# Optimization experiments

Measured on AMD Instinct MI355X. Metric: run time of the kernel, lower is better.

The kernel has to match this reference:

```python
import jax, jax.numpy as jnp
import numpy as np

DIST_THRESH = 150.0
ROW_EPS = 1e-6
BN_EPS = 1e-5


def setup_inputs() -> dict:
    key = jax.random.key(0)
    ks = jax.random.split(key, 6)
    B, N, T, D = 64, 64, 16, 512
    person_features = jax.random.normal(ks[0], (B, N, T, D), dtype=jnp.float32)
    # bboxes in pixel-ish units so the 150px threshold gives a mixed adjacency
    bboxes = jax.random.uniform(ks[1], (B, N, 4), dtype=jnp.float32) * 300.0
    w1 = jax.random.normal(ks[2], (D, D), dtype=jnp.float32) * (1.0 / np.sqrt(D))
    b1 = jax.random.normal(ks[3], (D,), dtype=jnp.float32) * 0.02
    w2 = jax.random.normal(ks[4], (D, D), dtype=jnp.float32) * (1.0 / np.sqrt(D))
    b2 = jax.random.normal(ks[5], (D,), dtype=jnp.float32) * 0.02
    g1 = jnp.ones((D,), jnp.float32); beta1 = jnp.zeros((D,), jnp.float32)
    g2 = jnp.ones((D,), jnp.float32); beta2 = jnp.zeros((D,), jnp.float32)
    return {"person_features": person_features, "bboxes": bboxes,
            "w1": w1, "b1": b1, "g1": g1, "beta1": beta1,
            "w2": w2, "b2": b2, "g2": g2, "beta2": beta2}


def _build_adjacency(bboxes):
    # centers: (B, N, 2) from x+w/2, y+h/2
    cx = bboxes[..., 0] + 0.5 * bboxes[..., 2]
    cy = bboxes[..., 1] + 0.5 * bboxes[..., 3]
    centers = jnp.stack([cx, cy], axis=-1)
    # pairwise distances (B, N, N), vectorized (replaces B*N*N python loop)
    diff = centers[:, :, None, :] - centers[:, None, :, :]
    dist = jnp.sqrt(jnp.sum(diff * diff, axis=-1))
    N = bboxes.shape[1]
    eye = jnp.eye(N, dtype=bboxes.dtype)
    off_diag = (eye[None] == 0.0)
    A = jnp.where((dist < DIST_THRESH) & off_diag, 1.0, 0.0) + eye[None]
    return A


def _stgcn(x, A, w, b, g, beta):
    # x: (B, N, C); A: (B, N, N)
    # torch: A_norm = A / (A.sum(dim=1 of A[i] -> axis=2) + eps)
    A_norm = A / (jnp.sum(A, axis=2, keepdims=True) + ROW_EPS)
    # x_graph = x[b].T @ A_norm[b]  -> (B, C, N)
    y = jnp.einsum('bnc,bnm->bcm', x, A_norm)
    # 1x1 conv == channel GEMM, bias added per out-channel
    y = jnp.einsum('oc,bcm->bom', w, y) + b[None, :, None]
    # BatchNorm2d in training mode: biased stats over (batch, spatial)
    mean = jnp.mean(y, axis=(0, 2), keepdims=True)
    var = jnp.mean(jnp.square(y - mean), axis=(0, 2), keepdims=True)
    y = (y - mean) / jnp.sqrt(var + BN_EPS)
    y = y * g[None, :, None] + beta[None, :, None]
    y = jax.nn.relu(y)
    return jnp.swapaxes(y, 1, 2)  # (B, N, C)


def reference(person_features, bboxes, w1, b1, g1, beta1, w2, b2, g2, beta2):
    A = _build_adjacency(bboxes)
    x = person_features[:, :, -1, :]  # (B, N, D) last frame
    h = _stgcn(x, A, w1, b1, g1, beta1)
    h = _stgcn(h, A, w2, b2, g2, beta2)
    # write enhanced features back into last timestep
    return person_features.at[:, :, -1, :].set(h)
```

## Files before the change

kernel.cpp:

```cpp
#include <hip/hip_runtime.h>
#include <hip/hip_bf16.h>


typedef __attribute__((ext_vector_type(8))) short short8;
typedef __attribute__((ext_vector_type(4))) float v4f;

#define DIST_THRESH 150.0f
#define ROW_EPS 1e-6f
#define BN_EPS 1e-5f

__device__ __forceinline__ ushort f2bf(float f) {
  union { __hip_bfloat16 h; ushort u; } cv;
  cv.h = __float2bfloat16(f);
  return cv.u;
}

__global__ __launch_bounds__(256) void k_copy_prep(const float4* __restrict__ in,
                                                   float4* __restrict__ out,
                                                   const float* __restrict__ w1,
                                                   const float* __restrict__ w2,
                                                   ushort* __restrict__ wb,
                                                   float* __restrict__ stats) {
  int blk = blockIdx.x;
  int t = threadIdx.x;
  if (blk < 8192) {
    size_t base = (size_t)blk * 1024 + t;
    float4 r0 = in[base];
    float4 r1 = in[base + 256];
    float4 r2 = in[base + 512];
    float4 r3 = in[base + 768];
    out[base] = r0;
    out[base + 256] = r1;
    out[base + 512] = r2;
    out[base + 768] = r3;
  } else {
    int idx = (blk - 8192) * 256 + t;
    float v = (idx < 262144) ? w1[idx] : w2[idx - 262144];
    wb[idx] = f2bf(v);
    if (idx < 2048) stats[idx] = 0.f;
  }
}

__global__ __launch_bounds__(256) void k_agg(const float* __restrict__ Xbase,
                                             int rowStride,
                                             const float* __restrict__ bb,
                                             const float* __restrict__ stats,
                                             const float* __restrict__ g,
                                             const float* __restrict__ beta,
                                             int applyBN,
                                             ushort* __restrict__ Z) {
  int b = blockIdx.x;
  int c0 = blockIdx.y * 128;
  int t = threadIdx.x;
  __shared__ float Xs[64][128];
  __shared__ float As[64][64];
  __shared__ float cxs[64], cys[64];
  __shared__ float scaleS[128], shiftS[128];
  __shared__ float rsum[64][4];
  __shared__ float invr[64];

  if (t < 64) {
    float4 v = *(const float4*)&bb[(size_t)(b * 64 + t) * 4];
    cxs[t] = v.x + 0.5f * v.z;
    cys[t] = v.y + 0.5f * v.w;
  }
  if (applyBN && t < 32) {
    int c = t * 4;
    float4 sm = *(const float4*)&stats[c0 + c];
    float4 sq = *(const float4*)&stats[512 + c0 + c];
    float4 gg = *(const float4*)&g[c0 + c];
    float4 bt = *(const float4*)&beta[c0 + c];
    const float inv = 1.0f / 4096.0f;
    float mean, var, sc;
    mean = sm.x * inv; var = sq.x * inv - mean * mean; sc = gg.x * rsqrtf(var + BN_EPS);
    scaleS[c] = sc; shiftS[c] = bt.x - mean * sc;
    mean = sm.y * inv; var = sq.y * inv - mean * mean; sc = gg.y * rsqrtf(var + BN_EPS);
    scaleS[c + 1] = sc; shiftS[c + 1] = bt.y - mean * sc;
    mean = sm.z * inv; var = sq.z * inv - mean * mean; sc = gg.z * rsqrtf(var + BN_EPS);
    scaleS[c + 2] = sc; shiftS[c + 2] = bt.z - mean * sc;
    mean = sm.w * inv; var = sq.w * inv - mean * mean; sc = gg.w * rsqrtf(var + BN_EPS);
    scaleS[c + 3] = sc; shiftS[c + 3] = bt.w - mean * sc;
  }
  __syncthreads();

  int an = t >> 2, aq = t & 3;
  float av[16];
  {
    float mycx = cxs[an], mycy = cys[an];
    float ps = 0.f;
#pragma unroll
    for (int j = 0; j < 16; ++j) {
      int m = aq * 16 + j;
      float dx = mycx - cxs[m], dy = mycy - cys[m];
      float d = sqrtf(dx * dx + dy * dy);
      float a = (m == an) ? 1.0f : ((d < DIST_THRESH) ? 1.0f : 0.0f);
      av[j] = a;
      ps += a;
    }
    rsum[an][aq] = ps;
  }

  const float* xb = Xbase + (size_t)b * 64 * rowStride;
  for (int i = t; i < 2048; i += 256) {
    int n = i >> 5, c4 = (i & 31) << 2;
    float4 x = *(const float4*)&xb[(size_t)n * rowStride + c0 + c4];
    if (applyBN) {
      x.x = fmaxf(x.x * scaleS[c4] + shiftS[c4], 0.f);
      x.y = fmaxf(x.y * scaleS[c4 + 1] + shiftS[c4 + 1], 0.f);
      x.z = fmaxf(x.z * scaleS[c4 + 2] + shiftS[c4 + 2], 0.f);
      x.w = fmaxf(x.w * scaleS[c4 + 3] + shiftS[c4 + 3], 0.f);
    }
    *(float4*)&Xs[n][c4] = x;
  }
  __syncthreads();

  if (t < 64)
    invr[t] = 1.0f / (rsum[t][0] + rsum[t][1] + rsum[t][2] + rsum[t][3] + ROW_EPS);
  __syncthreads();

  {
    float iv = invr[an];
#pragma unroll
    for (int j = 0; j < 16; ++j) As[an][aq * 16 + j] = av[j] * iv;
  }
  __syncthreads();

  int c4 = (t & 31) << 2;
  int m0 = (t >> 5) << 3;
  float4 acc[8];
#pragma unroll
  for (int i = 0; i < 8; ++i) acc[i] = make_float4(0.f, 0.f, 0.f, 0.f);

  for (int n = 0; n < 64; ++n) {
    float4 x = *(const float4*)&Xs[n][c4];
    float4 a0 = *(const float4*)&As[n][m0];
    float4 a1 = *(const float4*)&As[n][m0 + 4];
    float as[8] = {a0.x, a0.y, a0.z, a0.w, a1.x, a1.y, a1.z, a1.w};
#pragma unroll
    for (int i = 0; i < 8; ++i) {
      acc[i].x = fmaf(as[i], x.x, acc[i].x);
      acc[i].y = fmaf(as[i], x.y, acc[i].y);
      acc[i].z = fmaf(as[i], x.z, acc[i].z);
      acc[i].w = fmaf(as[i], x.w, acc[i].w);
    }
  }

  size_t zbase = (size_t)b * 64 * 512 + c0 + c4;
#pragma unroll
  for (int i = 0; i < 8; ++i) {
    int m = m0 + i;
    ushort4 zz;
    zz.x = f2bf(acc[i].x);
    zz.y = f2bf(acc[i].y);
    zz.z = f2bf(acc[i].z);
    zz.w = f2bf(acc[i].w);
    *(ushort4*)&Z[zbase + (size_t)m * 512] = zz;
  }
}

__global__ __launch_bounds__(256) void k_gemm(const ushort* __restrict__ Z,
                                              const ushort* __restrict__ W,
                                              const float* __restrict__ bias,
                                              float* __restrict__ Y,
                                              float* __restrict__ sum,
                                              float* __restrict__ sumsq) {
  __shared__ __align__(16) ushort Zs[64 * 40];
  __shared__ __align__(16) ushort Ws[64 * 40];
  __shared__ float redS[4][64], redQ[4][64];

  int t = threadIdx.x;
  int r0 = blockIdx.x * 64;
  int o0 = blockIdx.y * 64;
  int wv = t >> 6, lane = t & 63;
  int m = lane & 15, q = lane >> 4;

  v4f acc[4];
#pragma unroll
  for (int nf = 0; nf < 4; ++nf) acc[nf] = (v4f){0.f, 0.f, 0.f, 0.f};

  int srow = t >> 2, scg = (t & 3) << 3;
  const ushort* zp = &Z[(size_t)(r0 + srow) * 512 + scg];
  const ushort* wp = &W[(size_t)(o0 + srow) * 512 + scg];

  uint4 zv = *(const uint4*)zp;
  uint4 wvv = *(const uint4*)wp;

  for (int ks = 0; ks < 16; ++ks) {
    __syncthreads();
    *(uint4*)&Zs[srow * 40 + scg] = zv;
    *(uint4*)&Ws[srow * 40 + scg] = wvv;
    __syncthreads();

    if (ks < 15) {
      zv = *(const uint4*)(zp + (ks + 1) * 32);
      wvv = *(const uint4*)(wp + (ks + 1) * 32);
    }

    short8 a = *(const short8*)&Zs[(wv * 16 + m) * 40 + q * 8];
#pragma unroll
    for (int nf = 0; nf < 4; ++nf) {
      short8 bfr = *(const short8*)&Ws[(nf * 16 + m) * 40 + q * 8];
      acc[nf] = __builtin_amdgcn_mfma_f32_16x16x32_bf16(a, bfr, acc[nf], 0, 0, 0);
    }
  }

#pragma unroll
  for (int nf = 0; nf < 4; ++nf) {
    int col = o0 + nf * 16 + m;
    float bv = bias[col];
    float s = 0.f, s2 = 0.f;
#pragma unroll
    for (int reg = 0; reg < 4; ++reg) {
      int row = r0 + wv * 16 + q * 4 + reg;
      float y = acc[nf][reg] + bv;
      Y[(size_t)row * 512 + col] = y;
      s += y;
      s2 += y * y;
    }
    s += __shfl_xor(s, 16);
    s += __shfl_xor(s, 32);
    s2 += __shfl_xor(s2, 16);
    s2 += __shfl_xor(s2, 32);
    if (q == 0) {
      redS[wv][nf * 16 + m] = s;
      redQ[wv][nf * 16 + m] = s2;
    }
  }
  __syncthreads();
  if (t < 64) {
    float s = redS[0][t] + redS[1][t] + redS[2][t] + redS[3][t];
    float s2 = redQ[0][t] + redQ[1][t] + redQ[2][t] + redQ[3][t];
    atomicAdd(&sum[o0 + t], s);
    atomicAdd(&sumsq[o0 + t], s2);
  }
}

__global__ __launch_bounds__(256) void k_norm(const float* __restrict__ Y,
                                              const float* __restrict__ sum,
                                              const float* __restrict__ sumsq,
                                              const float* __restrict__ g,
                                              const float* __restrict__ beta,
                                              float* __restrict__ out) {
  int idx = blockIdx.x * 256 + threadIdx.x;
  int o = (idx & 127) << 2;
  int r = idx >> 7;
  float4 y = *(const float4*)&Y[(size_t)r * 512 + o];
  float4 sm = *(const float4*)&sum[o];
  float4 sq = *(const float4*)&sumsq[o];
  float4 gg = *(const float4*)&g[o];
  float4 bb = *(const float4*)&beta[o];
  const float inv = 1.0f / 4096.0f;
  float4 h;
  {
    float mean = sm.x * inv, var = sq.x * inv - mean * mean;
    h.x = fmaxf(gg.x * (y.x - mean) * rsqrtf(var + BN_EPS) + bb.x, 0.f);
  }
  {
    float mean = sm.y * inv, var = sq.y * inv - mean * mean;
    h.y = fmaxf(gg.y * (y.y - mean) * rsqrtf(var + BN_EPS) + bb.y, 0.f);
  }
  {
    float mean = sm.z * inv, var = sq.z * inv - mean * mean;
    h.z = fmaxf(gg.z * (y.z - mean) * rsqrtf(var + BN_EPS) + bb.z, 0.f);
  }
  {
    float mean = sm.w * inv, var = sq.w * inv - mean * mean;
    h.w = fmaxf(gg.w * (y.w - mean) * rsqrtf(var + BN_EPS) + bb.w, 0.f);
  }
  *(float4*)&out[((size_t)r * 16 + 15) * 512 + o] = h;
}

extern "C" void kernel_launch(void* const* d_in, const int* in_sizes, int n_in,
                              void* d_out, int out_size, void* d_ws, size_t ws_size,
                              hipStream_t stream) {
  const float* pf = (const float*)d_in[0];
  const float* bboxes = (const float*)d_in[1];
  const float* w1 = (const float*)d_in[2];
  const float* b1 = (const float*)d_in[3];
  const float* g1 = (const float*)d_in[4];
  const float* be1 = (const float*)d_in[5];
  const float* w2 = (const float*)d_in[6];
  const float* b2 = (const float*)d_in[7];
  const float* g2 = (const float*)d_in[8];
  const float* be2 = (const float*)d_in[9];
  float* out = (float*)d_out;

  ushort* wb = (ushort*)d_ws;
  ushort* Zb = wb + 524288;
  float* Yb = (float*)(Zb + 2097152);
  float* stats = Yb + 2097152;
  float* sum1 = stats;
  float* sq1 = stats + 512;
  float* sum2 = stats + 1024;
  float* sq2 = stats + 1536;

  k_copy_prep<<<10240, 256, 0, stream>>>((const float4*)pf, (float4*)out, w1, w2, wb, stats);

  k_agg<<<dim3(64, 4), 256, 0, stream>>>(pf + 7680, 8192, bboxes, stats, g1, be1, 0, Zb);
  k_gemm<<<dim3(64, 8), 256, 0, stream>>>(Zb, wb, b1, Yb, sum1, sq1);

  k_agg<<<dim3(64, 4), 256, 0, stream>>>(Yb, 512, bboxes, stats, g1, be1, 1, Zb);
  k_gemm<<<dim3(64, 8), 256, 0, stream>>>(Zb, wb + 262144, b2, Yb, sum2, sq2);

  k_norm<<<2048, 256, 0, stream>>>(Yb, sum2, sq2, g2, be2, out);
}
```

Measured before the change: 295.7 us.

## Fold feature copy and weight prep into compute kernels as extra blocks

Removes the standalone copy/prep kernel. Its 8192 copy slabs are split across the two aggregation and two GEMM launches as extra trailing blocks, and the bf16 weight conversion plus stats zeroing move into the first aggregation launch, now vectorised to float4. The goal is to overlap the bandwidth-bound copy of the feature tensor with the small, latency-bound graph and GEMM kernels, and to save one launch. The risk is that copy blocks inherit the compute kernels' large shared-memory footprint, which lowers their occupancy, and they compete with the compute blocks for bandwidth.

```diff
diff --git a/kernel.cpp b/kernel.cpp
--- a/kernel.cpp
+++ b/kernel.cpp
@@ -15,30 +15,18 @@
   return cv.u;
 }
 
-__global__ __launch_bounds__(256) void k_copy_prep(const float4* __restrict__ in,
-                                                   float4* __restrict__ out,
-                                                   const float* __restrict__ w1,
-                                                   const float* __restrict__ w2,
-                                                   ushort* __restrict__ wb,
-                                                   float* __restrict__ stats) {
-  int blk = blockIdx.x;
-  int t = threadIdx.x;
-  if (blk < 8192) {
-    size_t base = (size_t)blk * 1024 + t;
-    float4 r0 = in[base];
-    float4 r1 = in[base + 256];
-    float4 r2 = in[base + 512];
-    float4 r3 = in[base + 768];
-    out[base] = r0;
-    out[base + 256] = r1;
-    out[base + 512] = r2;
-    out[base + 768] = r3;
-  } else {
-    int idx = (blk - 8192) * 256 + t;
-    float v = (idx < 262144) ? w1[idx] : w2[idx - 262144];
-    wb[idx] = f2bf(v);
-    if (idx < 2048) stats[idx] = 0.f;
-  }
+__device__ __forceinline__ void copy_slab(const float4* __restrict__ in,
+                                          float4* __restrict__ out,
+                                          int blk, int t) {
+  size_t base = (size_t)blk * 1024 + t;
+  float4 r0 = in[base];
+  float4 r1 = in[base + 256];
+  float4 r2 = in[base + 512];
+  float4 r3 = in[base + 768];
+  out[base] = r0;
+  out[base + 256] = r1;
+  out[base + 512] = r2;
+  out[base + 768] = r3;
 }
 
 __global__ __launch_bounds__(256) void k_agg(const float* __restrict__ Xbase,
@@ -48,10 +36,38 @@
                                              const float* __restrict__ g,
                                              const float* __restrict__ beta,
                                              int applyBN,
-                                             ushort* __restrict__ Z) {
-  int b = blockIdx.x;
-  int c0 = blockIdx.y * 128;
+                                             ushort* __restrict__ Z,
+                                             const float4* __restrict__ in4,
+                                             float4* __restrict__ out4,
+                                             int copyBase,
+                                             int nonCopy,
+                                             const float* __restrict__ w1,
+                                             const float* __restrict__ w2,
+                                             ushort* __restrict__ wb,
+                                             float* __restrict__ statsZ) {
+  int id = blockIdx.x;
   int t = threadIdx.x;
+
+  if (id >= nonCopy) {
+    copy_slab(in4, out4, copyBase + (id - nonCopy), t);
+    return;
+  }
+  if (id >= 256) {
+    int i4 = (id - 256) * 256 + t;
+    float4 v = (i4 < 65536) ? *(const float4*)&w1[(size_t)i4 * 4]
+                            : *(const float4*)&w2[(size_t)(i4 - 65536) * 4];
+    ushort4 o;
+    o.x = f2bf(v.x);
+    o.y = f2bf(v.y);
+    o.z = f2bf(v.z);
+    o.w = f2bf(v.w);
+    *(ushort4*)&wb[(size_t)i4 * 4] = o;
+    if (i4 < 512) *(float4*)&statsZ[i4 * 4] = make_float4(0.f, 0.f, 0.f, 0.f);
+    return;
+  }
+
+  int b = id >> 2;
+  int c0 = (id & 3) << 7;
   __shared__ float Xs[64][128];
   __shared__ float As[64][64];
   __shared__ float cxs[64], cys[64];
@@ -163,14 +179,23 @@
                                               const float* __restrict__ bias,
                                               float* __restrict__ Y,
                                               float* __restrict__ sum,
-                                              float* __restrict__ sumsq) {
+                                              float* __restrict__ sumsq,
+                                              const float4* __restrict__ in4,
+                                              float4* __restrict__ out4,
+                                              int copyBase) {
+  int id = blockIdx.x;
+  int t = threadIdx.x;
+  if (id >= 512) {
+    copy_slab(in4, out4, copyBase + (id - 512), t);
+    return;
+  }
+
   __shared__ __align__(16) ushort Zs[64 * 40];
   __shared__ __align__(16) ushort Ws[64 * 40];
   __shared__ float redS[4][64], redQ[4][64];
 
-  int t = threadIdx.x;
-  int r0 = blockIdx.x * 64;
-  int o0 = blockIdx.y * 64;
+  int r0 = (id >> 3) << 6;
+  int o0 = (id & 7) << 6;
   int wv = t >> 6, lane = t & 63;
   int m = lane & 15, q = lane >> 4;
 
@@ -294,13 +319,18 @@
   float* sum2 = stats + 1024;
   float* sq2 = stats + 1536;
 
-  k_copy_prep<<<10240, 256, 0, stream>>>((const float4*)pf, (float4*)out, w1, w2, wb, stats);
-
-  k_agg<<<dim3(64, 4), 256, 0, stream>>>(pf + 7680, 8192, bboxes, stats, g1, be1, 0, Zb);
-  k_gemm<<<dim3(64, 8), 256, 0, stream>>>(Zb, wb, b1, Yb, sum1, sq1);
-
-  k_agg<<<dim3(64, 4), 256, 0, stream>>>(Yb, 512, bboxes, stats, g1, be1, 1, Zb);
-  k_gemm<<<dim3(64, 8), 256, 0, stream>>>(Zb, wb + 262144, b2, Yb, sum2, sq2);
-
+  const float4* in4 = (const float4*)pf;
+  float4* out4 = (float4*)out;
+
+  k_agg<<<256 + 512 + 2048, 256, 0, stream>>>(pf + 7680, 8192, bboxes, stats,
+                                              g1, be1, 0, Zb,
+                                              in4, out4, 0, 768, w1, w2, wb, stats);
+  k_gemm<<<512 + 2048, 256, 0, stream>>>(Zb, wb, b1, Yb, sum1, sq1,
+                                         in4, out4, 2048);
+  k_agg<<<256 + 2048, 256, 0, stream>>>(Yb, 512, bboxes, stats,
+                                        g1, be1, 1, Zb,
+                                        in4, out4, 4096, 256, w1, w2, wb, stats);
+  k_gemm<<<512 + 2048, 256, 0, stream>>>(Zb, wb + 262144, b2, Yb, sum2, sq2,
+                                         in4, out4, 6144);
   k_norm<<<2048, 256, 0, stream>>>(Yb, sum2, sq2, g2, be2, out);
 }
```

Result: faster. 280.2 us (-5.3%).

## Fuse pipeline into one cooperative persistent kernel overlapping the bulk copy

Applied to the files above, without the earlier changes.

All six launches are replaced by a single cooperative kernel with 512 blocks. Grid syncs separate the aggregation, GEMM and norm phases, and the large person_features copy is spread across the phases through atomic work-stealing counters so it overlaps the compute. The copy skips the last timestep, which the norm phase writes. This removes launch gaps and hides the memory-bound copy behind compute, at the cost of grid-sync overhead and the requirement that all blocks are co-resident. If the cooperative launch fails, it falls back to separate kernels.

```diff
diff --git a/kernel.cpp b/kernel.cpp
--- a/kernel.cpp
+++ b/kernel.cpp
@@ -1,5 +1,8 @@
 #include <hip/hip_runtime.h>
 #include <hip/hip_bf16.h>
+#include <hip/hip_cooperative_groups.h>
+
+namespace cg = cooperative_groups;
 
 
 typedef __attribute__((ext_vector_type(8))) short short8;
@@ -15,14 +18,358 @@
   return cv.u;
 }
 
-__global__ __launch_bounds__(256) void k_copy_prep(const float4* __restrict__ in,
-                                                   float4* __restrict__ out,
-                                                   const float* __restrict__ w1,
-                                                   const float* __restrict__ w2,
-                                                   ushort* __restrict__ wb,
-                                                   float* __restrict__ stats) {
-  int blk = blockIdx.x;
-  int t = threadIdx.x;
+struct AggShared {
+  float Xs[64][128];
+  float As[64][64];
+  float cxs[64], cys[64];
+  float scaleS[128], shiftS[128];
+  float rsum[64][4];
+  float invr[64];
+};
+struct GemmShared {
+  ushort Zs[64 * 40];
+  ushort Ws[64 * 40];
+  float redS[4][64], redQ[4][64];
+};
+union ShU { AggShared a; GemmShared g; };
+
+__device__ __forceinline__ void copy_chunk(const float4* __restrict__ in,
+                                           float4* __restrict__ out,
+                                           int c, int lane, bool skipT15) {
+  size_t base = (size_t)c * 256 + lane;
+  float4 r0 = in[base];
+  float4 r1 = in[base + 64];
+  float4 r2 = in[base + 128];
+  float4 r3 = in[base + 192];
+  out[base] = r0;
+  out[base + 64] = r1;
+  if (!skipT15) {
+    out[base + 128] = r2;
+    out[base + 192] = r3;
+  }
+}
+
+__device__ __forceinline__ void steal_copy(const float4* __restrict__ in,
+                                           float4* __restrict__ out,
+                                           int* __restrict__ ctr,
+                                           int base, int ngroups, int lane,
+                                           bool p4) {
+  for (;;) {
+    int i;
+    if (lane == 0) i = atomicAdd(ctr, 1);
+    i = __shfl(i, 0);
+    if (i >= ngroups) break;
+#pragma unroll
+    for (int k = 0; k < 8; ++k) {
+      int c = base + i * 8 + k;
+      copy_chunk(in, out, c, lane, p4 && ((c & 7) == 7));
+    }
+  }
+}
+
+__device__ __forceinline__ void prep_unit(int i4, const float* __restrict__ w1,
+                                          const float* __restrict__ w2,
+                                          ushort* __restrict__ wb) {
+  float4 v = (i4 < 65536) ? *(const float4*)&w1[(size_t)i4 * 4]
+                          : *(const float4*)&w2[(size_t)(i4 - 65536) * 4];
+  ushort4 o;
+  o.x = f2bf(v.x);
+  o.y = f2bf(v.y);
+  o.z = f2bf(v.z);
+  o.w = f2bf(v.w);
+  *(ushort4*)&wb[(size_t)i4 * 4] = o;
+}
+
+__device__ void agg_unit(int u, int t, const float* __restrict__ Xbase,
+                         int rowStride, const float* __restrict__ bb,
+                         const float* __restrict__ stats,
+                         const float* __restrict__ g,
+                         const float* __restrict__ beta, int applyBN,
+                         ushort* __restrict__ Z, AggShared& S) {
+  int b = u >> 2;
+  int c0 = (u & 3) << 7;
+
+  if (t < 64) {
+    float4 v = *(const float4*)&bb[(size_t)(b * 64 + t) * 4];
+    S.cxs[t] = v.x + 0.5f * v.z;
+    S.cys[t] = v.y + 0.5f * v.w;
+  }
+  if (applyBN && t < 32) {
+    int c = t * 4;
+    float4 sm = *(const float4*)&stats[c0 + c];
+    float4 sq = *(const float4*)&stats[512 + c0 + c];
+    float4 gg = *(const float4*)&g[c0 + c];
+    float4 bt = *(const float4*)&beta[c0 + c];
+    const float inv = 1.0f / 4096.0f;
+    float mean, var, sc;
+    mean = sm.x * inv; var = sq.x * inv - mean * mean; sc = gg.x * rsqrtf(var + BN_EPS);
+    S.scaleS[c] = sc; S.shiftS[c] = bt.x - mean * sc;
+    mean = sm.y * inv; var = sq.y * inv - mean * mean; sc = gg.y * rsqrtf(var + BN_EPS);
+    S.scaleS[c + 1] = sc; S.shiftS[c + 1] = bt.y - mean * sc;
+    mean = sm.z * inv; var = sq.z * inv - mean * mean; sc = gg.z * rsqrtf(var + BN_EPS);
+    S.scaleS[c + 2] = sc; S.shiftS[c + 2] = bt.z - mean * sc;
+    mean = sm.w * inv; var = sq.w * inv - mean * mean; sc = gg.w * rsqrtf(var + BN_EPS);
+    S.scaleS[c + 3] = sc; S.shiftS[c + 3] = bt.w - mean * sc;
+  }
+  __syncthreads();
+
+  int an = t >> 2, aq = t & 3;
+  float av[16];
+  {
+    float mycx = S.cxs[an], mycy = S.cys[an];
+    float ps = 0.f;
+#pragma unroll
+    for (int j = 0; j < 16; ++j) {
+      int m = aq * 16 + j;
+      float dx = mycx - S.cxs[m], dy = mycy - S.cys[m];
+      float d = sqrtf(dx * dx + dy * dy);
+      float a = (m == an) ? 1.0f : ((d < DIST_THRESH) ? 1.0f : 0.0f);
+      av[j] = a;
+      ps += a;
+    }
+    S.rsum[an][aq] = ps;
+  }
+
+  const float* xb = Xbase + (size_t)b * 64 * rowStride;
+  for (int i = t; i < 2048; i += 256) {
+    int n = i >> 5, c4 = (i & 31) << 2;
+    float4 x = *(const float4*)&xb[(size_t)n * rowStride + c0 + c4];
+    if (applyBN) {
+      x.x = fmaxf(x.x * S.scaleS[c4] + S.shiftS[c4], 0.f);
+      x.y = fmaxf(x.y * S.scaleS[c4 + 1] + S.shiftS[c4 + 1], 0.f);
+      x.z = fmaxf(x.z * S.scaleS[c4 + 2] + S.shiftS[c4 + 2], 0.f);
+      x.w = fmaxf(x.w * S.scaleS[c4 + 3] + S.shiftS[c4 + 3], 0.f);
+    }
+    *(float4*)&S.Xs[n][c4] = x;
+  }
+  __syncthreads();
+
+  if (t < 64)
+    S.invr[t] = 1.0f / (S.rsum[t][0] + S.rsum[t][1] + S.rsum[t][2] + S.rsum[t][3] + ROW_EPS);
+  __syncthreads();
+
+  {
+    float iv = S.invr[an];
+#pragma unroll
+    for (int j = 0; j < 16; ++j) S.As[an][aq * 16 + j] = av[j] * iv;
+  }
+  __syncthreads();
+
+  int c4 = (t & 31) << 2;
+  int m0 = (t >> 5) << 3;
+  float4 acc[8];
+#pragma unroll
+  for (int i = 0; i < 8; ++i) acc[i] = make_float4(0.f, 0.f, 0.f, 0.f);
+
+  for (int n = 0; n < 64; ++n) {
+    float4 x = *(const float4*)&S.Xs[n][c4];
+    float4 a0 = *(const float4*)&S.As[n][m0];
+    float4 a1 = *(const float4*)&S.As[n][m0 + 4];
+    float as[8] = {a0.x, a0.y, a0.z, a0.w, a1.x, a1.y, a1.z, a1.w};
+#pragma unroll
+    for (int i = 0; i < 8; ++i) {
+      acc[i].x = fmaf(as[i], x.x, acc[i].x);
+      acc[i].y = fmaf(as[i], x.y, acc[i].y);
+      acc[i].z = fmaf(as[i], x.z, acc[i].z);
+      acc[i].w = fmaf(as[i], x.w, acc[i].w);
+    }
+  }
+
+  size_t zbase = (size_t)b * 64 * 512 + c0 + c4;
+#pragma unroll
+  for (int i = 0; i < 8; ++i) {
+    int m = m0 + i;
+    ushort4 zz;
+    zz.x = f2bf(acc[i].x);
+    zz.y = f2bf(acc[i].y);
+    zz.z = f2bf(acc[i].z);
+    zz.w = f2bf(acc[i].w);
+    *(ushort4*)&Z[zbase + (size_t)m * 512] = zz;
+  }
+  __syncthreads();
+}
+
+__device__ void gemm_unit(int u, int t, const ushort* __restrict__ Z,
+                          const ushort* __restrict__ W,
+                          const float* __restrict__ bias,
+                          float* __restrict__ Y, float* __restrict__ sum,
+                          float* __restrict__ sumsq, GemmShared& S) {
+  int r0 = (u >> 3) << 6;
+  int o0 = (u & 7) << 6;
+  int wv = t >> 6, lane = t & 63;
+  int m = lane & 15, q = lane >> 4;
+
+  v4f acc[4];
+#pragma unroll
+  for (int nf = 0; nf < 4; ++nf) acc[nf] = (v4f){0.f, 0.f, 0.f, 0.f};
+
+  int srow = t >> 2, scg = (t & 3) << 3;
+  const ushort* zp = &Z[(size_t)(r0 + srow) * 512 + scg];
+  const ushort* wp = &W[(size_t)(o0 + srow) * 512 + scg];
+
+  uint4 zv = *(const uint4*)zp;
+  uint4 wvv = *(const uint4*)wp;
+
+  for (int ks = 0; ks < 16; ++ks) {
+    __syncthreads();
+    *(uint4*)&S.Zs[srow * 40 + scg] = zv;
+    *(uint4*)&S.Ws[srow * 40 + scg] = wvv;
+    __syncthreads();
+
+    if (ks < 15) {
+      zv = *(const uint4*)(zp + (ks + 1) * 32);
+      wvv = *(const uint4*)(wp + (ks + 1) * 32);
+    }
+
+    short8 a = *(const short8*)&S.Zs[(wv * 16 + m) * 40 + q * 8];
+#pragma unroll
+    for (int nf = 0; nf < 4; ++nf) {
+      short8 bfr = *(const short8*)&S.Ws[(nf * 16 + m) * 40 + q * 8];
+      acc[nf] = __builtin_amdgcn_mfma_f32_16x16x32_bf16(a, bfr, acc[nf], 0, 0, 0);
+    }
+  }
+
+#pragma unroll
+  for (int nf = 0; nf < 4; ++nf) {
+    int col = o0 + nf * 16 + m;
+    float bv = bias[col];
+    float s = 0.f, s2 = 0.f;
+#pragma unroll
+    for (int reg = 0; reg < 4; ++reg) {
+      int row = r0 + wv * 16 + q * 4 + reg;
+      float y = acc[nf][reg] + bv;
+      Y[(size_t)row * 512 + col] = y;
+      s += y;
+      s2 += y * y;
+    }
+    s += __shfl_xor(s, 16);
+    s += __shfl_xor(s, 32);
+    s2 += __shfl_xor(s2, 16);
+    s2 += __shfl_xor(s2, 32);
+    if (q == 0) {
+      S.redS[wv][nf * 16 + m] = s;
+      S.redQ[wv][nf * 16 + m] = s2;
+    }
+  }
+  __syncthreads();
+  if (t < 64) {
+    float s = S.redS[0][t] + S.redS[1][t] + S.redS[2][t] + S.redS[3][t];
+    float s2 = S.redQ[0][t] + S.redQ[1][t] + S.redQ[2][t] + S.redQ[3][t];
+    atomicAdd(&sum[o0 + t], s);
+    atomicAdd(&sumsq[o0 + t], s2);
+  }
+  __syncthreads();
+}
+
+__device__ __forceinline__ void norm_unit(int unit, int t,
+                                          const float* __restrict__ Y,
+                                          const float* __restrict__ sum,
+                                          const float* __restrict__ sumsq,
+                                          const float* __restrict__ g,
+                                          const float* __restrict__ beta,
+                                          float* __restrict__ out) {
+  int idx = unit * 256 + t;
+  int o = (idx & 127) << 2;
+  int r = idx >> 7;
+  float4 y = *(const float4*)&Y[(size_t)r * 512 + o];
+  float4 sm = *(const float4*)&sum[o];
+  float4 sq = *(const float4*)&sumsq[o];
+  float4 gg = *(const float4*)&g[o];
+  float4 bb = *(const float4*)&beta[o];
+  const float inv = 1.0f / 4096.0f;
+  float4 h;
+  {
+    float mean = sm.x * inv, var = sq.x * inv - mean * mean;
+    h.x = fmaxf(gg.x * (y.x - mean) * rsqrtf(var + BN_EPS) + bb.x, 0.f);
+  }
+  {
+    float mean = sm.y * inv, var = sq.y * inv - mean * mean;
+    h.y = fmaxf(gg.y * (y.y - mean) * rsqrtf(var + BN_EPS) + bb.y, 0.f);
+  }
+  {
+    float mean = sm.z * inv, var = sq.z * inv - mean * mean;
+    h.z = fmaxf(gg.z * (y.z - mean) * rsqrtf(var + BN_EPS) + bb.z, 0.f);
+  }
+  {
+    float mean = sm.w * inv, var = sq.w * inv - mean * mean;
+    h.w = fmaxf(gg.w * (y.w - mean) * rsqrtf(var + BN_EPS) + bb.w, 0.f);
+  }
+  *(float4*)&out[((size_t)r * 16 + 15) * 512 + o] = h;
+}
+
+__global__ __launch_bounds__(256, 2) void k_fused(
+    const float* __restrict__ pf, const float* __restrict__ bboxes,
+    const float* __restrict__ w1, const float* __restrict__ b1,
+    const float* __restrict__ g1, const float* __restrict__ be1,
+    const float* __restrict__ w2, const float* __restrict__ b2,
+    const float* __restrict__ g2, const float* __restrict__ be2,
+    float* __restrict__ out, ushort* __restrict__ wb, ushort* __restrict__ Zb,
+    float* __restrict__ Yb, float* __restrict__ stats, int* __restrict__ ctr) {
+  cg::grid_group grid = cg::this_grid();
+  __shared__ ShU sh;
+  int bid = blockIdx.x, t = threadIdx.x, lane = t & 63;
+  const float4* in4 = (const float4*)pf;
+  float4* out4 = (float4*)out;
+  float* sum1 = stats;
+  float* sq1 = stats + 512;
+  float* sum2 = stats + 1024;
+  float* sq2 = stats + 1536;
+
+  if (bid < 256) {
+    agg_unit(bid, t, pf + 7680, 8192, bboxes, stats, g1, be1, 0, Zb, sh.a);
+  } else {
+    int pb = bid - 256;
+#pragma unroll
+    for (int u = 0; u < 2; ++u) prep_unit((pb * 2 + u) * 256 + t, w1, w2, wb);
+    if (pb == 0) {
+      for (int i = t; i < 512; i += 256)
+        ((float4*)stats)[i] = make_float4(0.f, 0.f, 0.f, 0.f);
+      if (t < 8) ctr[t] = 0;
+    }
+    int cbase = pb * 24 + (t >> 6) * 6;
+#pragma unroll
+    for (int s = 0; s < 6; ++s) copy_chunk(in4, out4, cbase + s, lane, false);
+  }
+  __threadfence();
+  grid.sync();
+
+  if (bid < 256) {
+    gemm_unit(bid * 2, t, Zb, wb, b1, Yb, sum1, sq1, sh.g);
+    gemm_unit(bid * 2 + 1, t, Zb, wb, b1, Yb, sum1, sq1, sh.g);
+  }
+  steal_copy(in4, out4, &ctr[1], 6144, 1024, lane, false);
+  __threadfence();
+  grid.sync();
+
+  if (bid < 256) agg_unit(bid, t, Yb, 512, bboxes, stats, g1, be1, 1, Zb, sh.a);
+  steal_copy(in4, out4, &ctr[2], 14336, 1024, lane, false);
+  __threadfence();
+  grid.sync();
+
+  if (bid < 256) {
+    gemm_unit(bid * 2, t, Zb, wb + 262144, b2, Yb, sum2, sq2, sh.g);
+    gemm_unit(bid * 2 + 1, t, Zb, wb + 262144, b2, Yb, sum2, sq2, sh.g);
+  }
+  steal_copy(in4, out4, &ctr[3], 22528, 1024, lane, false);
+  __threadfence();
+  grid.sync();
+
+  if (bid >= 256) {
+    int pb = bid - 256;
+#pragma unroll
+    for (int u = 0; u < 8; ++u)
+      norm_unit(pb * 8 + u, t, Yb, sum2, sq2, g2, be2, out);
+  }
+  steal_copy(in4, out4, &ctr[4], 30720, 256, lane, true);
+}
+
+__global__ __launch_bounds__(256) void k_copy_prep_fb(const float4* __restrict__ in,
+                                                      float4* __restrict__ out,
+                                                      const float* __restrict__ w1,
+                                                      const float* __restrict__ w2,
+                                                      ushort* __restrict__ wb,
+                                                      float* __restrict__ stats) {
+  int blk = blockIdx.x, t = threadIdx.x;
   if (blk < 8192) {
     size_t base = (size_t)blk * 1024 + t;
     float4 r0 = in[base];
@@ -34,240 +381,40 @@
     out[base + 512] = r2;
     out[base + 768] = r3;
   } else {
-    int idx = (blk - 8192) * 256 + t;
-    float v = (idx < 262144) ? w1[idx] : w2[idx - 262144];
-    wb[idx] = f2bf(v);
-    if (idx < 2048) stats[idx] = 0.f;
-  }
-}
-
-__global__ __launch_bounds__(256) void k_agg(const float* __restrict__ Xbase,
-                                             int rowStride,
-                                             const float* __restrict__ bb,
-                                             const float* __restrict__ stats,
-                                             const float* __restrict__ g,
-                                             const float* __restrict__ beta,
-                                             int applyBN,
-                                             ushort* __restrict__ Z) {
-  int b = blockIdx.x;
-  int c0 = blockIdx.y * 128;
-  int t = threadIdx.x;
-  __shared__ float Xs[64][128];
-  __shared__ float As[64][64];
-  __shared__ float cxs[64], cys[64];
-  __shared__ float scaleS[128], shiftS[128];
-  __shared__ float rsum[64][4];
-  __shared__ float invr[64];
-
-  if (t < 64) {
-    float4 v = *(const float4*)&bb[(size_t)(b * 64 + t) * 4];
-    cxs[t] = v.x + 0.5f * v.z;
-    cys[t] = v.y + 0.5f * v.w;
-  }
-  if (applyBN && t < 32) {
-    int c = t * 4;
-    float4 sm = *(const float4*)&stats[c0 + c];
-    float4 sq = *(const float4*)&stats[512 + c0 + c];
-    float4 gg = *(const float4*)&g[c0 + c];
-    float4 bt = *(const float4*)&beta[c0 + c];
-    const float inv = 1.0f / 4096.0f;
-    float mean, var, sc;
-    mean = sm.x * inv; var = sq.x * inv - mean * mean; sc = gg.x * rsqrtf(var + BN_EPS);
-    scaleS[c] = sc; shiftS[c] = bt.x - mean * sc;
-    mean = sm.y * inv; var = sq.y * inv - mean * mean; sc = gg.y * rsqrtf(var + BN_EPS);
-    scaleS[c + 1] = sc; shiftS[c + 1] = bt.y - mean * sc;
-    mean = sm.z * inv; var = sq.z * inv - mean * mean; sc = gg.z * rsqrtf(var + BN_EPS);
-    scaleS[c + 2] = sc; shiftS[c + 2] = bt.z - mean * sc;
-    mean = sm.w * inv; var = sq.w * inv - mean * mean; sc = gg.w * rsqrtf(var + BN_EPS);
-    scaleS[c + 3] = sc; shiftS[c + 3] = bt.w - mean * sc;
-  }
-  __syncthreads();
-
-  int an = t >> 2, aq = t & 3;
-  float av[16];
-  {
-    float mycx = cxs[an], mycy = cys[an];
-    float ps = 0.f;
-#pragma unroll
-    for (int j = 0; j < 16; ++j) {
-      int m = aq * 16 + j;
-      float dx = mycx - cxs[m], dy = mycy - cys[m];
-      float d = sqrtf(dx * dx + dy * dy);
-      float a = (m == an) ? 1.0f : ((d < DIST_THRESH) ? 1.0f : 0.0f);
-      av[j] = a;
-      ps += a;
-    }
-    rsum[an][aq] = ps;
-  }
-
-  const float* xb = Xbase + (size_t)b * 64 * rowStride;
-  for (int i = t; i < 2048; i += 256) {
-    int n = i >> 5, c4 = (i & 31) << 2;
-    float4 x = *(const float4*)&xb[(size_t)n * rowStride + c0 + c4];
-    if (applyBN) {
-      x.x = fmaxf(x.x * scaleS[c4] + shiftS[c4], 0.f);
-      x.y = fmaxf(x.y * scaleS[c4 + 1] + shiftS[c4 + 1], 0.f);
-      x.z = fmaxf(x.z * scaleS[c4 + 2] + shiftS[c4 + 2], 0.f);
-      x.w = fmaxf(x.w * scaleS[c4 + 3] + shiftS[c4 + 3], 0.f);
-    }
-    *(float4*)&Xs[n][c4] = x;
-  }
-  __syncthreads();
-
-  if (t < 64)
-    invr[t] = 1.0f / (rsum[t][0] + rsum[t][1] + rsum[t][2] + rsum[t][3] + ROW_EPS);
-  __syncthreads();
-
-  {
-    float iv = invr[an];
-#pragma unroll
-    for (int j = 0; j < 16; ++j) As[an][aq * 16 + j] = av[j] * iv;
-  }
-  __syncthreads();
-
-  int c4 = (t & 31) << 2;
-  int m0 = (t >> 5) << 3;
-  float4 acc[8];
-#pragma unroll
-  for (int i = 0; i < 8; ++i) acc[i] = make_float4(0.f, 0.f, 0.f, 0.f);
-
-  for (int n = 0; n < 64; ++n) {
-    float4 x = *(const float4*)&Xs[n][c4];
-    float4 a0 = *(const float4*)&As[n][m0];
-    float4 a1 = *(const float4*)&As[n][m0 + 4];
-    float as[8] = {a0.x, a0.y, a0.z, a0.w, a1.x, a1.y, a1.z, a1.w};
-#pragma unroll
-    for (int i = 0; i < 8; ++i) {
-      acc[i].x = fmaf(as[i], x.x, acc[i].x);
-      acc[i].y = fmaf(as[i], x.y, acc[i].y);
-      acc[i].z = fmaf(as[i], x.z, acc[i].z);
-      acc[i].w = fmaf(as[i], x.w, acc[i].w);
-    }
-  }
-
-  size_t zbase = (size_t)b * 64 * 512 + c0 + c4;
-#pragma unroll
-  for (int i = 0; i < 8; ++i) {
-    int m = m0 + i;
-    ushort4 zz;
-    zz.x = f2bf(acc[i].x);
-    zz.y = f2bf(acc[i].y);
-    zz.z = f2bf(acc[i].z);
-    zz.w = f2bf(acc[i].w);
-    *(ushort4*)&Z[zbase + (size_t)m * 512] = zz;
-  }
-}
-
-__global__ __launch_bounds__(256) void k_gemm(const ushort* __restrict__ Z,
-                                              const ushort* __restrict__ W,
-                                              const float* __restrict__ bias,
-                                              float* __restrict__ Y,
-                                              float* __restrict__ sum,
-                                              float* __restrict__ sumsq) {
-  __shared__ __align__(16) ushort Zs[64 * 40];
-  __shared__ __align__(16) ushort Ws[64 * 40];
-  __shared__ float redS[4][64], redQ[4][64];
-
-  int t = threadIdx.x;
-  int r0 = blockIdx.x * 64;
-  int o0 = blockIdx.y * 64;
-  int wv = t >> 6, lane = t & 63;
-  int m = lane & 15, q = lane >> 4;
-
-  v4f acc[4];
-#pragma unroll
-  for (int nf = 0; nf < 4; ++nf) acc[nf] = (v4f){0.f, 0.f, 0.f, 0.f};
-
-  int srow = t >> 2, scg = (t & 3) << 3;
-  const ushort* zp = &Z[(size_t)(r0 + srow) * 512 + scg];
-  const ushort* wp = &W[(size_t)(o0 + srow) * 512 + scg];
-
-  uint4 zv = *(const uint4*)zp;
-  uint4 wvv = *(const uint4*)wp;
-
-  for (int ks = 0; ks < 16; ++ks) {
-    __syncthreads();
-    *(uint4*)&Zs[srow * 40 + scg] = zv;
-    *(uint4*)&Ws[srow * 40 + scg] = wvv;
-    __syncthreads();
-
-    if (ks < 15) {
-      zv = *(const uint4*)(zp + (ks + 1) * 32);
-      wvv = *(const uint4*)(wp + (ks + 1) * 32);
-    }
-
-    short8 a = *(const short8*)&Zs[(wv * 16 + m) * 40 + q * 8];
-#pragma unroll
-    for (int nf = 0; nf < 4; ++nf) {
-      short8 bfr = *(const short8*)&Ws[(nf * 16 + m) * 40 + q * 8];
-      acc[nf] = __builtin_amdgcn_mfma_f32_16x16x32_bf16(a, bfr, acc[nf], 0, 0, 0);
-    }
-  }
-
-#pragma unroll
-  for (int nf = 0; nf < 4; ++nf) {
-    int col = o0 + nf * 16 + m;
-    float bv = bias[col];
-    float s = 0.f, s2 = 0.f;
-#pragma unroll
-    for (int reg = 0; reg < 4; ++reg) {
-      int row = r0 + wv * 16 + q * 4 + reg;
-      float y = acc[nf][reg] + bv;
-      Y[(size_t)row * 512 + col] = y;
-      s += y;
-      s2 += y * y;
-    }
-    s += __shfl_xor(s, 16);
-    s += __shfl_xor(s, 32);
-    s2 += __shfl_xor(s2, 16);
-    s2 += __shfl_xor(s2, 32);
-    if (q == 0) {
-      redS[wv][nf * 16 + m] = s;
-      redQ[wv][nf * 16 + m] = s2;
-    }
-  }
-  __syncthreads();
-  if (t < 64) {
-    float s = redS[0][t] + redS[1][t] + redS[2][t] + redS[3][t];
-    float s2 = redQ[0][t] + redQ[1][t] + redQ[2][t] + redQ[3][t];
-    atomicAdd(&sum[o0 + t], s);
-    atomicAdd(&sumsq[o0 + t], s2);
-  }
-}
-
-__global__ __launch_bounds__(256) void k_norm(const float* __restrict__ Y,
-                                              const float* __restrict__ sum,
-                                              const float* __restrict__ sumsq,
-                                              const float* __restrict__ g,
-                                              const float* __restrict__ beta,
-                                              float* __restrict__ out) {
-  int idx = blockIdx.x * 256 + threadIdx.x;
-  int o = (idx & 127) << 2;
-  int r = idx >> 7;
-  float4 y = *(const float4*)&Y[(size_t)r * 512 + o];
-  float4 sm = *(const float4*)&sum[o];
-  float4 sq = *(const float4*)&sumsq[o];
-  float4 gg = *(const float4*)&g[o];
-  float4 bb = *(const float4*)&beta[o];
-  const float inv = 1.0f / 4096.0f;
-  float4 h;
-  {
-    float mean = sm.x * inv, var = sq.x * inv - mean * mean;
-    h.x = fmaxf(gg.x * (y.x - mean) * rsqrtf(var + BN_EPS) + bb.x, 0.f);
-  }
-  {
-    float mean = sm.y * inv, var = sq.y * inv - mean * mean;
-    h.y = fmaxf(gg.y * (y.y - mean) * rsqrtf(var + BN_EPS) + bb.y, 0.f);
-  }
-  {
-    float mean = sm.z * inv, var = sq.z * inv - mean * mean;
-    h.z = fmaxf(gg.z * (y.z - mean) * rsqrtf(var + BN_EPS) + bb.z, 0.f);
-  }
-  {
-    float mean = sm.w * inv, var = sq.w * inv - mean * mean;
-    h.w = fmaxf(gg.w * (y.w - mean) * rsqrtf(var + BN_EPS) + bb.w, 0.f);
-  }
-  *(float4*)&out[((size_t)r * 16 + 15) * 512 + o] = h;
+    prep_unit((blk - 8192) * 256 + t, w1, w2, wb);
+    if (blk == 8192) {
+      for (int i = t; i < 512; i += 256)
+        ((float4*)stats)[i] = make_float4(0.f, 0.f, 0.f, 0.f);
+    }
+  }
+}
+__global__ __launch_bounds__(256) void k_agg_fb(const float* __restrict__ Xbase,
+                                                int rowStride,
+                                                const float* __restrict__ bb,
+                                                const float* __restrict__ stats,
+                                                const float* __restrict__ g,
+                                                const float* __restrict__ beta,
+                                                int applyBN,
+                                                ushort* __restrict__ Z) {
+  __shared__ AggShared S;
+  agg_unit(blockIdx.x, threadIdx.x, Xbase, rowStride, bb, stats, g, beta, applyBN, Z, S);
+}
+__global__ __launch_bounds__(256) void k_gemm_fb(const ushort* __restrict__ Z,
+                                                 const ushort* __restrict__ W,
+                                                 const float* __restrict__ bias,
+                                                 float* __restrict__ Y,
+                                                 float* __restrict__ sum,
+                                                 float* __restrict__ sumsq) {
+  __shared__ GemmShared S;
+  gemm_unit(blockIdx.x, threadIdx.x, Z, W, bias, Y, sum, sumsq, S);
+}
+__global__ __launch_bounds__(256) void k_norm_fb(const float* __restrict__ Y,
+                                                 const float* __restrict__ sum,
+                                                 const float* __restrict__ sumsq,
+                                                 const float* __restrict__ g,
+                                                 const float* __restrict__ beta,
+                                                 float* __restrict__ out) {
+  norm_unit(blockIdx.x, threadIdx.x, Y, sum, sumsq, g, beta, out);
 }
 
 extern "C" void kernel_launch(void* const* d_in, const int* in_sizes, int n_in,
@@ -289,18 +436,26 @@
   ushort* Zb = wb + 524288;
   float* Yb = (float*)(Zb + 2097152);
   float* stats = Yb + 2097152;
+  int* ctr = (int*)(stats + 2048);
   float* sum1 = stats;
   float* sq1 = stats + 512;
   float* sum2 = stats + 1024;
   float* sq2 = stats + 1536;
 
-  k_copy_prep<<<10240, 256, 0, stream>>>((const float4*)pf, (float4*)out, w1, w2, wb, stats);
-
-  k_agg<<<dim3(64, 4), 256, 0, stream>>>(pf + 7680, 8192, bboxes, stats, g1, be1, 0, Zb);
-  k_gemm<<<dim3(64, 8), 256, 0, stream>>>(Zb, wb, b1, Yb, sum1, sq1);
-
-  k_agg<<<dim3(64, 4), 256, 0, stream>>>(Yb, 512, bboxes, stats, g1, be1, 1, Zb);
-  k_gemm<<<dim3(64, 8), 256, 0, stream>>>(Zb, wb + 262144, b2, Yb, sum2, sq2);
-
-  k_norm<<<2048, 256, 0, stream>>>(Yb, sum2, sq2, g2, be2, out);
-}
+  void* args[16] = {(void*)&pf,  (void*)&bboxes, (void*)&w1,  (void*)&b1,
+                    (void*)&g1,  (void*)&be1,    (void*)&w2,  (void*)&b2,
+                    (void*)&g2,  (void*)&be2,    (void*)&out, (void*)&wb,
+                    (void*)&Zb,  (void*)&Yb,     (void*)&stats, (void*)&ctr};
+  hipError_t e = hipLaunchCooperativeKernel((const void*)k_fused, dim3(512),
+                                            dim3(256), args, 0, stream);
+  if (e != hipSuccess) {
+    (void)hipGetLastError();
+    k_copy_prep_fb<<<8704, 256, 0, stream>>>((const float4*)pf, (float4*)out,
+                                             w1, w2, wb, stats);
+    k_agg_fb<<<256, 256, 0, stream>>>(pf + 7680, 8192, bboxes, stats, g1, be1, 0, Zb);
+    k_gemm_fb<<<512, 256, 0, stream>>>(Zb, wb, b1, Yb, sum1, sq1);
+    k_agg_fb<<<256, 256, 0, stream>>>(Yb, 512, bboxes, stats, g1, be1, 1, Zb);
+    k_gemm_fb<<<512, 256, 0, stream>>>(Zb, wb + 262144, b2, Yb, sum2, sq2);
+    k_norm_fb<<<2048, 256, 0, stream>>>(Yb, sum2, sq2, g2, be2, out);
+  }
+}
```

Measured after the change: 826.2 us. 2.79x slower.
